# Kernel tuning notes

Hardware: AMD Instinct MI355X
Metric: run time of the kernel (lower is better)

The kernel has to match this reference:

```python
import jax, jax.numpy as jnp
import numpy as np
from jax import lax

B, L, C, K = 8, 4096, 128, 7
NORM_FACTOR = 1.0


def setup_inputs() -> dict:
    key = jax.random.key(0)
    kx, kw = jax.random.split(key)
    x = jax.random.normal(kx, (B, L, C), dtype=jnp.float32)
    # lecun_normal: std = 1/sqrt(fan_in); flax computes fan_in over leading dims -> C*C here is
    # not the point for a correctness baseline; use std = 1/sqrt(C*K) as a reasonable scale.
    weights = jax.random.normal(kw, (C, C, K), dtype=jnp.float32) / np.sqrt(C * K).astype(np.float32)
    return {"x": x, "weights": weights}


def reference(x, weights):
    batch, seq, ch = x.shape
    k = weights.shape[2]
    lp = seq - k + 1  # valid-padding output length
    # unfold: (B, C, L) -> (B, C*K, Lp) -> (B, K, C, Lp)
    patches = lax.conv_general_dilated_patches(
        jnp.transpose(x, (0, 2, 1)), filter_shape=(k,), window_strides=(1,), padding=((0, 0),)
    )
    xp = jnp.transpose(jnp.reshape(patches, (batch, ch, k, lp)), (0, 2, 1, 3))  # (B,K,C,Lp)
    # dynamic kernel from the last Lp positions of the raw input
    # einsum 'abc,dcg->adbg': (B,Lp,C) x (C,C,K) -> (B,C,Lp,K)
    w = jnp.einsum('blc,dck->bdlk', x[:, -lp:, :], weights)
    w = jnp.tanh(jnp.transpose(w, (0, 3, 1, 2)) / NORM_FACTOR)  # (B,K,C,Lp)
    out = jnp.sum(xp * w, axis=1)  # (B,C,Lp)
    return jnp.transpose(out, (0, 2, 1))  # (B,Lp,C)
```

## Files before the change

### kernel.cpp

```cpp
#include <hip/hip_runtime.h>
#include <hip/hip_bf16.h>
#include <math.h>

namespace {

constexpr int B_ = 8, L_ = 4096, C_ = 128, K_ = 7;
constexpr int LP = L_ - K_ + 1;
constexpr int CK = C_ * K_;

typedef __attribute__((ext_vector_type(8))) _Float16 half8v;
typedef __attribute__((ext_vector_type(4))) float f32x4;

__device__ __forceinline__ float fast_tanh(float v) {
    float a = fabsf(v);
    float e = __expf(2.0f * a);
    float t = fmaf(-2.0f, __builtin_amdgcn_rcpf(e + 1.0f), 1.0f);
    unsigned s = __float_as_uint(v) & 0x80000000u;
    return __uint_as_float(__float_as_uint(t) | s);
}

__global__ __launch_bounds__(256, 2) void sidechain_fused(
        const float* __restrict__ x, const float* __restrict__ W,
        float* __restrict__ out) {
    __shared__ _Float16 Bs[7 * 16 * C_];

    const int tid = threadIdx.x;
    const int b  = blockIdx.x >> 4;
    const int l0 = (blockIdx.x & 15) * 256;
    const int d0 = blockIdx.y * 16;

    const float* xb = x + (size_t)b * (L_ * C_);

    {
        const int dl = tid >> 4;
        const int g  = tid & 15;
        const int gp = g ^ dl;
        const float* wp = W + (size_t)(d0 + dl) * CK + g * 56;
        float wbuf[56];
#pragma unroll
        for (int i = 0; i < 14; ++i)
            *reinterpret_cast<float4*>(&wbuf[i * 4]) =
                *reinterpret_cast<const float4*>(&wp[i * 4]);
#pragma unroll
        for (int k = 0; k < 7; ++k) {
            half8v h;
#pragma unroll
            for (int c = 0; c < 8; ++c) h[c] = (_Float16)wbuf[c * 7 + k];
            *reinterpret_cast<half8v*>(&Bs[(k * 16 + dl) * C_ + gp * 8]) = h;
        }
    }
    __syncthreads();

    const int wv   = tid >> 6;
    const int lane = tid & 63;
    const int rA   = lane & 15;
    const int kg   = lane >> 4;
    const int dcol = d0 + rA;

#pragma unroll 1
    for (int half = 0; half < 2; ++half) {
        half8v A[2][4];
#pragma unroll
        for (int m = 0; m < 2; ++m) {
            int mt = half * 2 + m;
            int r = l0 + 6 + wv * 64 + mt * 16 + rA;
            if (r > L_ - 1) r = L_ - 1;
            const float* xr = xb + (size_t)r * C_;
#pragma unroll
            for (int ks = 0; ks < 4; ++ks) {
                const float* p = xr + ks * 32 + kg * 8;
                const float4 f0 = *reinterpret_cast<const float4*>(p);
                const float4 f1 = *reinterpret_cast<const float4*>(p + 4);
                half8v h;
                h[0] = (_Float16)f0.x; h[1] = (_Float16)f0.y;
                h[2] = (_Float16)f0.z; h[3] = (_Float16)f0.w;
                h[4] = (_Float16)f1.x; h[5] = (_Float16)f1.y;
                h[6] = (_Float16)f1.z; h[7] = (_Float16)f1.w;
                A[m][ks] = h;
            }
        }

        float xv[2][10];
#pragma unroll
        for (int m = 0; m < 2; ++m) {
            int mt = half * 2 + m;
            int base = l0 + wv * 64 + mt * 16 + kg * 4;
#pragma unroll
            for (int r2 = 0; r2 < 10; ++r2) {
                int row = base + r2;
                if (row > L_ - 1) row = L_ - 1;
                xv[m][r2] = xb[(size_t)row * C_ + dcol];
            }
        }

        f32x4 oacc[2];
#pragma unroll
        for (int m = 0; m < 2; ++m) oacc[m] = (f32x4)(0.0f);

#pragma unroll
        for (int nt = 0; nt < 7; ++nt) {
            f32x4 acc[2];
#pragma unroll
            for (int m = 0; m < 2; ++m) acc[m] = (f32x4)(0.0f);
#pragma unroll
            for (int ks = 0; ks < 4; ++ks) {
                int gp2 = (ks * 4 + kg) ^ rA;
                const half8v Bf = *reinterpret_cast<const half8v*>(&Bs[(nt * 16 + rA) * C_ + gp2 * 8]);
#pragma unroll
                for (int m = 0; m < 2; ++m)
                    acc[m] = __builtin_amdgcn_mfma_f32_16x16x32_f16(A[m][ks], Bf, acc[m], 0, 0, 0);
            }
#pragma unroll
            for (int m = 0; m < 2; ++m)
#pragma unroll
                for (int r = 0; r < 4; ++r)
                    oacc[m][r] = fmaf(xv[m][r + nt], fast_tanh(acc[m][r]), oacc[m][r]);
        }

#pragma unroll
        for (int m = 0; m < 2; ++m) {
            int mt = half * 2 + m;
#pragma unroll
            for (int r = 0; r < 4; ++r) {
                int l = l0 + wv * 64 + mt * 16 + kg * 4 + r;
                if (l < LP) out[((size_t)b * LP + l) * C_ + dcol] = oacc[m][r];
            }
        }
    }
}

}

extern "C" void kernel_launch(void* const* d_in, const int* in_sizes, int n_in,
                              void* d_out, int out_size, void* d_ws, size_t ws_size,
                              hipStream_t stream) {
    const float* x = (const float*)d_in[0];
    const float* w = (const float*)d_in[1];
    float* out     = (float*)d_out;
    (void)d_ws; (void)ws_size; (void)in_sizes; (void)n_in; (void)out_size;

    dim3 grid(B_ * 16, C_ / 16);
    sidechain_fused<<<grid, dim3(256), 0, stream>>>(x, w, out);
}
```

Baseline: 90.88 us.

## Software-pipeline per-tile loads with compute and split MFMA accumulator chains

Replaces the two-half loop with a double-buffered schedule: the A fragments and x values for the next 16-row tile are loaded while the current tile runs its MFMAs and tanh epilogue, so global-load latency can hide behind compute. Each tile's MFMA reduction is split into two independent accumulators, shortening the dependent chain. tanh drops the abs/sign handling and uses 1-2/(exp(2v)+1) directly. Large negative inputs still give the right limit, large positive ones overflow exp and land near 1, and register pressure changes.

```diff
diff --git a/kernel.cpp b/kernel.cpp
--- a/kernel.cpp
+++ b/kernel.cpp
@@ -1,5 +1,4 @@
 #include <hip/hip_runtime.h>
-#include <hip/hip_bf16.h>
 #include <math.h>
 
 namespace {
@@ -12,11 +11,8 @@
 typedef __attribute__((ext_vector_type(4))) float f32x4;
 
 __device__ __forceinline__ float fast_tanh(float v) {
-    float a = fabsf(v);
-    float e = __expf(2.0f * a);
-    float t = fmaf(-2.0f, __builtin_amdgcn_rcpf(e + 1.0f), 1.0f);
-    unsigned s = __float_as_uint(v) & 0x80000000u;
-    return __uint_as_float(__float_as_uint(t) | s);
+    float e = __expf(2.0f * v);
+    return fmaf(-2.0f, __builtin_amdgcn_rcpf(e + 1.0f), 1.0f);
 }
 
 __global__ __launch_bounds__(256, 2) void sidechain_fused(
@@ -28,7 +24,6 @@
     const int b  = blockIdx.x >> 4;
     const int l0 = (blockIdx.x & 15) * 256;
     const int d0 = blockIdx.y * 16;
-
     const float* xb = x + (size_t)b * (L_ * C_);
 
     {
@@ -56,77 +51,70 @@
     const int rA   = lane & 15;
     const int kg   = lane >> 4;
     const int dcol = d0 + rA;
+    const int rowA0 = l0 + 6 + wv * 64 + rA;
+    const int rowX0 = l0 + wv * 64 + kg * 4;
 
-#pragma unroll 1
-    for (int half = 0; half < 2; ++half) {
-        half8v A[2][4];
+    auto loadA = [&](int mt, half8v (&A)[4]) {
+        int r = rowA0 + mt * 16;
+        if (r > L_ - 1) r = L_ - 1;
+        const float* xr = xb + (size_t)r * C_;
 #pragma unroll
-        for (int m = 0; m < 2; ++m) {
-            int mt = half * 2 + m;
-            int r = l0 + 6 + wv * 64 + mt * 16 + rA;
-            if (r > L_ - 1) r = L_ - 1;
-            const float* xr = xb + (size_t)r * C_;
+        for (int ks = 0; ks < 4; ++ks) {
+            const float* p = xr + ks * 32 + kg * 8;
+            const float4 f0 = *reinterpret_cast<const float4*>(p);
+            const float4 f1 = *reinterpret_cast<const float4*>(p + 4);
+            half8v h;
+            h[0] = (_Float16)f0.x; h[1] = (_Float16)f0.y;
+            h[2] = (_Float16)f0.z; h[3] = (_Float16)f0.w;
+            h[4] = (_Float16)f1.x; h[5] = (_Float16)f1.y;
+            h[6] = (_Float16)f1.z; h[7] = (_Float16)f1.w;
+            A[ks] = h;
+        }
+    };
+    auto loadXV = [&](int mt, float (&xv)[10]) {
+        int base = rowX0 + mt * 16;
 #pragma unroll
-            for (int ks = 0; ks < 4; ++ks) {
-                const float* p = xr + ks * 32 + kg * 8;
-                const float4 f0 = *reinterpret_cast<const float4*>(p);
-                const float4 f1 = *reinterpret_cast<const float4*>(p + 4);
-                half8v h;
-                h[0] = (_Float16)f0.x; h[1] = (_Float16)f0.y;
-                h[2] = (_Float16)f0.z; h[3] = (_Float16)f0.w;
-                h[4] = (_Float16)f1.x; h[5] = (_Float16)f1.y;
-                h[6] = (_Float16)f1.z; h[7] = (_Float16)f1.w;
-                A[m][ks] = h;
-            }
+        for (int r2 = 0; r2 < 10; ++r2) {
+            int row = base + r2;
+            if (row > L_ - 1) row = L_ - 1;
+            xv[r2] = xb[(size_t)row * C_ + dcol];
         }
-
-        float xv[2][10];
-#pragma unroll
-        for (int m = 0; m < 2; ++m) {
-            int mt = half * 2 + m;
-            int base = l0 + wv * 64 + mt * 16 + kg * 4;
-#pragma unroll
-            for (int r2 = 0; r2 < 10; ++r2) {
-                int row = base + r2;
-                if (row > L_ - 1) row = L_ - 1;
-                xv[m][r2] = xb[(size_t)row * C_ + dcol];
-            }
-        }
-
-        f32x4 oacc[2];
-#pragma unroll
-        for (int m = 0; m < 2; ++m) oacc[m] = (f32x4)(0.0f);
-
+    };
+    auto compute = [&](int mt, const half8v (&A)[4], const float (&xv)[10]) {
+        f32x4 oacc = (f32x4)(0.0f);
 #pragma unroll
         for (int nt = 0; nt < 7; ++nt) {
-            f32x4 acc[2];
+            f32x4 a0 = (f32x4)(0.0f), a1 = (f32x4)(0.0f);
 #pragma unroll
-            for (int m = 0; m < 2; ++m) acc[m] = (f32x4)(0.0f);
-#pragma unroll
-            for (int ks = 0; ks < 4; ++ks) {
-                int gp2 = (ks * 4 + kg) ^ rA;
-                const half8v Bf = *reinterpret_cast<const half8v*>(&Bs[(nt * 16 + rA) * C_ + gp2 * 8]);
-#pragma unroll
-                for (int m = 0; m < 2; ++m)
-                    acc[m] = __builtin_amdgcn_mfma_f32_16x16x32_f16(A[m][ks], Bf, acc[m], 0, 0, 0);
+            for (int ks = 0; ks < 4; ks += 2) {
+                int g0 = (ks * 4 + kg) ^ rA;
+                int g1 = ((ks + 1) * 4 + kg) ^ rA;
+                const half8v B0 = *reinterpret_cast<const half8v*>(&Bs[(nt * 16 + rA) * C_ + g0 * 8]);
+                const half8v B1 = *reinterpret_cast<const half8v*>(&Bs[(nt * 16 + rA) * C_ + g1 * 8]);
+                a0 = __builtin_amdgcn_mfma_f32_16x16x32_f16(A[ks],     B0, a0, 0, 0, 0);
+                a1 = __builtin_amdgcn_mfma_f32_16x16x32_f16(A[ks + 1], B1, a1, 0, 0, 0);
             }
 #pragma unroll
-            for (int m = 0; m < 2; ++m)
+            for (int r = 0; r < 4; ++r)
+                oacc[r] = fmaf(xv[r + nt], fast_tanh(a0[r] + a1[r]), oacc[r]);
+        }
 #pragma unroll
-                for (int r = 0; r < 4; ++r)
-                    oacc[m][r] = fmaf(xv[m][r + nt], fast_tanh(acc[m][r]), oacc[m][r]);
+        for (int r = 0; r < 4; ++r) {
+            int l = rowX0 + mt * 16 + r;
+            if (l < LP) out[((size_t)b * LP + l) * C_ + dcol] = oacc[r];
         }
+    };
 
-#pragma unroll
-        for (int m = 0; m < 2; ++m) {
-            int mt = half * 2 + m;
-#pragma unroll
-            for (int r = 0; r < 4; ++r) {
-                int l = l0 + wv * 64 + mt * 16 + kg * 4 + r;
-                if (l < LP) out[((size_t)b * LP + l) * C_ + dcol] = oacc[m][r];
-            }
-        }
-    }
+    half8v A0[4], A1[4];
+    float  xv0[10], xv1[10];
+    loadA(0, A0); loadXV(0, xv0);
+    loadA(1, A1); loadXV(1, xv1);
+    compute(0, A0, xv0);
+    loadA(2, A0); loadXV(2, xv0);
+    compute(1, A1, xv1);
+    loadA(3, A1); loadXV(3, xv1);
+    compute(2, A0, xv0);
+    compute(3, A1, xv1);
 }
 
 }
```

Result: faster. 87.95 us (-3.2%).

## Pre-convert x to fp16 in workspace and split MFMA accumulator chains

Applied to the files above, without the earlier changes.

Adds a separate kernel that converts x to fp16 in the workspace, so the fused kernel loads A fragments as half8 directly instead of reading fp32 and converting per block. Each x row is reread by the 8 channel-tile blocks, so the aim is to halve that repeated A traffic and cut conversion ALU work, at the cost of an extra launch plus one full fp32 read and fp16 write of x. The fused kernel also splits each MFMA accumulation into two independent chains to shorten dependency stalls. The tanh drops its abs/sign trick, which risks inf/NaN handling for large negative inputs. An fp32 fallback path is kept for when the workspace is too small.

```diff
diff --git a/kernel.cpp b/kernel.cpp
--- a/kernel.cpp
+++ b/kernel.cpp
@@ -1,5 +1,4 @@
 #include <hip/hip_runtime.h>
-#include <hip/hip_bf16.h>
 #include <math.h>
 
 namespace {
@@ -7,29 +6,41 @@
 constexpr int B_ = 8, L_ = 4096, C_ = 128, K_ = 7;
 constexpr int LP = L_ - K_ + 1;
 constexpr int CK = C_ * K_;
+constexpr size_t NX = (size_t)B_ * L_ * C_;
 
 typedef __attribute__((ext_vector_type(8))) _Float16 half8v;
 typedef __attribute__((ext_vector_type(4))) float f32x4;
 
 __device__ __forceinline__ float fast_tanh(float v) {
-    float a = fabsf(v);
-    float e = __expf(2.0f * a);
-    float t = fmaf(-2.0f, __builtin_amdgcn_rcpf(e + 1.0f), 1.0f);
-    unsigned s = __float_as_uint(v) & 0x80000000u;
-    return __uint_as_float(__float_as_uint(t) | s);
+    float e = __expf(2.0f * v);
+    return fmaf(-2.0f, __builtin_amdgcn_rcpf(e + 1.0f), 1.0f);
 }
 
+__global__ void convert_x(const float* __restrict__ x, _Float16* __restrict__ xh) {
+    size_t i = (size_t)(blockIdx.x * 256 + threadIdx.x) * 8;
+    if (i >= NX) return;
+    const float4 f0 = *reinterpret_cast<const float4*>(&x[i]);
+    const float4 f1 = *reinterpret_cast<const float4*>(&x[i + 4]);
+    half8v h;
+    h[0] = (_Float16)f0.x; h[1] = (_Float16)f0.y;
+    h[2] = (_Float16)f0.z; h[3] = (_Float16)f0.w;
+    h[4] = (_Float16)f1.x; h[5] = (_Float16)f1.y;
+    h[6] = (_Float16)f1.z; h[7] = (_Float16)f1.w;
+    *reinterpret_cast<half8v*>(&xh[i]) = h;
+}
+
+template <bool PRECONV>
 __global__ __launch_bounds__(256, 2) void sidechain_fused(
-        const float* __restrict__ x, const float* __restrict__ W,
-        float* __restrict__ out) {
+        const float* __restrict__ x, const _Float16* __restrict__ xh,
+        const float* __restrict__ W, float* __restrict__ out) {
     __shared__ _Float16 Bs[7 * 16 * C_];
 
     const int tid = threadIdx.x;
     const int b  = blockIdx.x >> 4;
     const int l0 = (blockIdx.x & 15) * 256;
     const int d0 = blockIdx.y * 16;
-
-    const float* xb = x + (size_t)b * (L_ * C_);
+    const float*    xb  = x  + (size_t)b * (L_ * C_);
+    const _Float16* xhb = xh + (size_t)b * (L_ * C_);
 
     {
         const int dl = tid >> 4;
@@ -56,35 +67,39 @@
     const int rA   = lane & 15;
     const int kg   = lane >> 4;
     const int dcol = d0 + rA;
+    const int rowA0 = l0 + 6 + wv * 64 + rA;
+    const int rowX0 = l0 + wv * 64 + kg * 4;
 
 #pragma unroll 1
     for (int half = 0; half < 2; ++half) {
         half8v A[2][4];
+        float  xv[2][10];
 #pragma unroll
         for (int m = 0; m < 2; ++m) {
             int mt = half * 2 + m;
-            int r = l0 + 6 + wv * 64 + mt * 16 + rA;
+            int r = rowA0 + mt * 16;
             if (r > L_ - 1) r = L_ - 1;
-            const float* xr = xb + (size_t)r * C_;
+            if (PRECONV) {
+                const _Float16* xr = xhb + (size_t)r * C_;
 #pragma unroll
-            for (int ks = 0; ks < 4; ++ks) {
-                const float* p = xr + ks * 32 + kg * 8;
-                const float4 f0 = *reinterpret_cast<const float4*>(p);
-                const float4 f1 = *reinterpret_cast<const float4*>(p + 4);
-                half8v h;
-                h[0] = (_Float16)f0.x; h[1] = (_Float16)f0.y;
-                h[2] = (_Float16)f0.z; h[3] = (_Float16)f0.w;
-                h[4] = (_Float16)f1.x; h[5] = (_Float16)f1.y;
-                h[6] = (_Float16)f1.z; h[7] = (_Float16)f1.w;
-                A[m][ks] = h;
+                for (int ks = 0; ks < 4; ++ks)
+                    A[m][ks] = *reinterpret_cast<const half8v*>(xr + ks * 32 + kg * 8);
+            } else {
+                const float* xr = xb + (size_t)r * C_;
+#pragma unroll
+                for (int ks = 0; ks < 4; ++ks) {
+                    const float* p = xr + ks * 32 + kg * 8;
+                    const float4 f0 = *reinterpret_cast<const float4*>(p);
+                    const float4 f1 = *reinterpret_cast<const float4*>(p + 4);
+                    half8v h;
+                    h[0] = (_Float16)f0.x; h[1] = (_Float16)f0.y;
+                    h[2] = (_Float16)f0.z; h[3] = (_Float16)f0.w;
+                    h[4] = (_Float16)f1.x; h[5] = (_Float16)f1.y;
+                    h[6] = (_Float16)f1.z; h[7] = (_Float16)f1.w;
+                    A[m][ks] = h;
+                }
             }
-        }
-
-        float xv[2][10];
-#pragma unroll
-        for (int m = 0; m < 2; ++m) {
-            int mt = half * 2 + m;
-            int base = l0 + wv * 64 + mt * 16 + kg * 4;
+            int base = rowX0 + mt * 16;
 #pragma unroll
             for (int r2 = 0; r2 < 10; ++r2) {
                 int row = base + r2;
@@ -94,27 +109,31 @@
         }
 
         f32x4 oacc[2];
-#pragma unroll
-        for (int m = 0; m < 2; ++m) oacc[m] = (f32x4)(0.0f);
+        oacc[0] = (f32x4)(0.0f); oacc[1] = (f32x4)(0.0f);
 
 #pragma unroll
         for (int nt = 0; nt < 7; ++nt) {
-            f32x4 acc[2];
+            f32x4 a0[2], a1[2];
+            a0[0] = (f32x4)(0.0f); a0[1] = (f32x4)(0.0f);
+            a1[0] = (f32x4)(0.0f); a1[1] = (f32x4)(0.0f);
+            const _Float16* brow = &Bs[(nt * 16 + rA) * C_];
 #pragma unroll
-            for (int m = 0; m < 2; ++m) acc[m] = (f32x4)(0.0f);
+            for (int kp = 0; kp < 4; kp += 2) {
+                int g0 = (kp * 4 + kg) ^ rA;
+                int g1 = ((kp + 1) * 4 + kg) ^ rA;
+                const half8v B0 = *reinterpret_cast<const half8v*>(brow + g0 * 8);
+                const half8v B1 = *reinterpret_cast<const half8v*>(brow + g1 * 8);
 #pragma unroll
-            for (int ks = 0; ks < 4; ++ks) {
-                int gp2 = (ks * 4 + kg) ^ rA;
-                const half8v Bf = *reinterpret_cast<const half8v*>(&Bs[(nt * 16 + rA) * C_ + gp2 * 8]);
-#pragma unroll
-                for (int m = 0; m < 2; ++m)
-                    acc[m] = __builtin_amdgcn_mfma_f32_16x16x32_f16(A[m][ks], Bf, acc[m], 0, 0, 0);
+                for (int m = 0; m < 2; ++m) {
+                    a0[m] = __builtin_amdgcn_mfma_f32_16x16x32_f16(A[m][kp],     B0, a0[m], 0, 0, 0);
+                    a1[m] = __builtin_amdgcn_mfma_f32_16x16x32_f16(A[m][kp + 1], B1, a1[m], 0, 0, 0);
+                }
             }
 #pragma unroll
             for (int m = 0; m < 2; ++m)
 #pragma unroll
                 for (int r = 0; r < 4; ++r)
-                    oacc[m][r] = fmaf(xv[m][r + nt], fast_tanh(acc[m][r]), oacc[m][r]);
+                    oacc[m][r] = fmaf(xv[m][r + nt], fast_tanh(a0[m][r] + a1[m][r]), oacc[m][r]);
         }
 
 #pragma unroll
@@ -122,7 +141,7 @@
             int mt = half * 2 + m;
 #pragma unroll
             for (int r = 0; r < 4; ++r) {
-                int l = l0 + wv * 64 + mt * 16 + kg * 4 + r;
+                int l = rowX0 + mt * 16 + r;
                 if (l < LP) out[((size_t)b * LP + l) * C_ + dcol] = oacc[m][r];
             }
         }
@@ -137,8 +156,15 @@
     const float* x = (const float*)d_in[0];
     const float* w = (const float*)d_in[1];
     float* out     = (float*)d_out;
-    (void)d_ws; (void)ws_size; (void)in_sizes; (void)n_in; (void)out_size;
+    (void)in_sizes; (void)n_in; (void)out_size;
 
     dim3 grid(B_ * 16, C_ / 16);
-    sidechain_fused<<<grid, dim3(256), 0, stream>>>(x, w, out);
+    const size_t need = NX * sizeof(_Float16);
+    if (ws_size >= need) {
+        _Float16* xh = (_Float16*)d_ws;
+        convert_x<<<dim3((int)(NX / 8 / 256)), dim3(256), 0, stream>>>(x, xh);
+        sidechain_fused<true><<<grid, dim3(256), 0, stream>>>(x, xh, w, out);
+    } else {
+        sidechain_fused<false><<<grid, dim3(256), 0, stream>>>(x, nullptr, w, out);
+    }
 }
```

After: 106.2 us. 16.8% more time.
